# Kernel tuning notes

Hardware: AMD Instinct MI355X
Metric: run time of the kernel (lower is better)

## Reference

```python
import jax, jax.numpy as jnp
import numpy as np

LAMDA = 0.001


def setup_inputs() -> dict:
    key = jax.random.key(0)
    k1, k2 = jax.random.split(key)
    embeddings = jax.random.normal(k1, (256, 1, 256, 256), dtype=jnp.float32)
    labels = jax.random.randint(k2, (256,), 0, 8, dtype=jnp.int64)
    return {"embeddings": embeddings, "labels": labels, "epoch": 1}


def _offdiag(M, b):
    # Remove the diagonal of a (b, b) matrix -> (b, b-1), same trick as torch code:
    # flatten()[1:].view(b-1, b+1)[:, :-1].reshape(b, b-1)
    return M.reshape(-1)[1:].reshape(b - 1, b + 1)[:, :-1].reshape(b, b - 1)


def _psd(embeddings):
    x = embeddings[:, 0]                      # (b, h, w), requires c == 1
    h, w = x.shape[1], x.shape[2]
    k = h * w
    dft = jnp.fft.fft2(x)                     # (b, h, w) complex
    avgpsd = jnp.mean((dft * jnp.conj(dft)).real, axis=0)   # (h, w)
    # log of (geometric mean / arithmetic mean) style flatness measure
    return jnp.clip(jnp.sum(jnp.log(avgpsd)) / k - jnp.log(jnp.sum(avgpsd) / k), 0.0, 100.0)


def reference(embeddings, labels, epoch):
    b = embeddings.shape[0]
    loss = -LAMDA * epoch * _psd(embeddings)

    e = embeddings.reshape(b, -1)             # (b, d)
    sq = jnp.sum(e * e, axis=1)               # (b,)
    d2 = sq[:, None] + sq[None, :] - 2.0 * (e @ e.T)   # squared pairwise distances
    d2 = jnp.maximum(d2, 0.0)
    D = jnp.where(d2 > 0, jnp.sqrt(jnp.where(d2 > 0, d2, 1.0)), 0.0)  # safe sqrt

    Doff = _offdiag(D, b)                     # (b, b-1)
    sm = jax.nn.softmax(-Doff, axis=1)        # (b, b-1)

    Loff = _offdiag(jnp.broadcast_to(labels[None, :], (b, b)), b)  # labels[j != i]
    mask = Loff == labels[:, None]            # positives per row
    probs = jnp.sum(jnp.where(mask, sm, 0.0), axis=1)  # (b,)

    loss = loss + jnp.sum(-jnp.log(probs)) / 200.0
    return loss
```

## Files before the change

### kernel.cpp

```cpp
#include <hip/hip_runtime.h>
#include <hip/hip_bf16.h>
#include <math.h>

#define NROW 256
#define DIM  65536
#define LSTR 40
#define PSP2 32832

typedef __attribute__((ext_vector_type(8))) short short8;
typedef __attribute__((ext_vector_type(4))) float f32x4;
typedef unsigned int       u32t;
typedef unsigned long long u64t;

__device__ __forceinline__ float bf2f(ushort h) {
    u32t u = ((u32t)h) << 16;
    return __builtin_bit_cast(float, u);
}
__device__ __forceinline__ u32t pk2(float lo, float hi) {
    __hip_bfloat162 h = __float22bfloat162_rn(make_float2(lo, hi));
    u32t r; __builtin_memcpy(&r, &h, 4); return r;
}

__device__ __forceinline__ int gpos2(int i, int j) {
    const int mh  = i >> 7, il = i & 127;
    const int wid  = ((il >> 6) << 2) | (j >> 6);
    const int lane = (((il >> 2) & 3) << 4) | (j & 15);
    const int q = ((wid << 6) | lane) * 64
                + (((((il >> 4) & 3) << 2) | ((j >> 4) & 3)) << 2) + (il & 3);
    return mh * 32768 + q;
}

__global__ __launch_bounds__(512, 4) void gemm_k(const float* __restrict__ E,
                                                 ushort* __restrict__ part) {
    const int b   = blockIdx.x;
    const int x   = b & 7;
    const int mh  = (b >> 3) & 1;
    const int s   = x * 32 + (b >> 4);

    const int tid  = threadIdx.x;
    const int lane = tid & 63;
    const int wid  = tid >> 6;
    const int wr   = wid >> 2;
    const int wc   = wid & 3;
    const int r15  = lane & 15;
    const int kgi  = lane >> 4;

    __shared__ ushort es[2][NROW][LSTR];

    const int row  = tid >> 1;
    const int half = tid & 1;
    const size_t kbase = (size_t)s * 256;

    f32x4 acc[4][4];
    #pragma unroll
    for (int m = 0; m < 4; ++m)
        #pragma unroll
        for (int n = 0; n < 4; ++n) acc[m][n] = (f32x4){0.f, 0.f, 0.f, 0.f};

    auto LOADC = [&](int c, float4* v) {
        const float* p = E + ((size_t)row << 16) + kbase + c * 32 + half * 16;
        #pragma unroll
        for (int u = 0; u < 4; ++u) v[u] = *(const float4*)(p + u * 4);
    };
    auto WRITEC = [&](int buf, const float4* v) {
        #pragma unroll
        for (int u = 0; u < 4; ++u) {
            uint2 wv;
            wv.x = pk2(v[u].x, v[u].y);
            wv.y = pk2(v[u].z, v[u].w);
            *(uint2*)&es[buf][row][half * 16 + u * 4] = wv;
        }
    };

    float4 v0[4];
    LOADC(0, v0);
    WRITEC(0, v0);

    #pragma unroll
    for (int c = 0; c < 8; ++c) {
        __syncthreads();
        float4 vn[4];
        if (c < 7) LOADC(c + 1, vn);
        const int ko = kgi * 8;
        short8 af[4], bfr[4];
        #pragma unroll
        for (int m = 0; m < 4; ++m)
            af[m] = *(const short8*)&es[c & 1][mh * 128 + wr * 64 + m * 16 + r15][ko];
        #pragma unroll
        for (int n = 0; n < 4; ++n)
            bfr[n] = *(const short8*)&es[c & 1][wc * 64 + n * 16 + r15][ko];
        #pragma unroll
        for (int m = 0; m < 4; ++m)
            #pragma unroll
            for (int n = 0; n < 4; ++n)
                acc[m][n] = __builtin_amdgcn_mfma_f32_16x16x32_bf16(
                    af[m], bfr[n], acc[m][n], 0, 0, 0);
        if (c < 7) WRITEC((c + 1) & 1, vn);
    }

    ushort* pp = part + (size_t)(s * 2 + mh) * PSP2 + (size_t)tid * 64;
    #pragma unroll
    for (int m = 0; m < 4; ++m)
        #pragma unroll
        for (int n = 0; n < 4; n += 2) {
            uint4 q;
            q.x = pk2(acc[m][n][0],     acc[m][n][1]);
            q.y = pk2(acc[m][n][2],     acc[m][n][3]);
            q.z = pk2(acc[m][n + 1][0], acc[m][n + 1][1]);
            q.w = pk2(acc[m][n + 1][2], acc[m][n + 1][3]);
            *(uint4*)(pp + ((m << 2) | n) * 4) = q;
        }
}

__global__ __launch_bounds__(256) void reduce_k(const ushort* __restrict__ part,
                                                float* __restrict__ Gh,
                                                u64t* __restrict__ acc,
                                                u32t* __restrict__ cnt) {
    if (blockIdx.x == 0 && threadIdx.x == 0) { *acc = 0ull; *cnt = 0u; }

    const int w  = blockIdx.x & 255;
    const int h  = blockIdx.x >> 8;
    const int mh = w >> 7;
    const int q0 = (w & 127) * 256;
    const int t = threadIdx.x, l = t & 63, sg = t >> 6;

    const ushort* base = part + (size_t)((h * 128 + sg) * 2 + mh) * PSP2
                              + q0 + l * 4;

    uint2 r[32];
    #pragma unroll
    for (int u = 0; u < 32; ++u)
        r[u] = *(const uint2*)(base + (size_t)(8 * u) * PSP2);

    float a0 = 0.f, a1 = 0.f, a2 = 0.f, a3 = 0.f;
    #pragma unroll
    for (int u = 0; u < 32; ++u) {
        a0 += bf2f((ushort)(r[u].x & 0xffffu));
        a1 += bf2f((ushort)(r[u].x >> 16));
        a2 += bf2f((ushort)(r[u].y & 0xffffu));
        a3 += bf2f((ushort)(r[u].y >> 16));
    }
    __shared__ float sh[4][256];
    sh[sg][l * 4 + 0] = a0; sh[sg][l * 4 + 1] = a1;
    sh[sg][l * 4 + 2] = a2; sh[sg][l * 4 + 3] = a3;
    __syncthreads();
    Gh[(size_t)h * 65536 + w * 256 + t] =
        (sh[0][t] + sh[1][t]) + (sh[2][t] + sh[3][t]);
}

__global__ __launch_bounds__(256) void row_loss_k(const float* __restrict__ Gh,
                                                  const int* __restrict__ labels,
                                                  u64t* __restrict__ acc,
                                                  u32t* __restrict__ cnt,
                                                  float* __restrict__ out) {
    const int i = blockIdx.x;
    const int j = threadIdx.x;

    const int pii = gpos2(i, i), pjj = gpos2(j, j), pij = gpos2(i, j);
    const float Gii = Gh[pii] + Gh[65536 + pii];
    const float Gjj = Gh[pjj] + Gh[65536 + pjj];
    const float Gij = Gh[pij] + Gh[65536 + pij];
    const float d2 = fmaxf(Gii + Gjj - 2.0f * Gij, 0.0f);
    const bool diag = (j == i);
    const float sc = diag ? -3.0e38f : -sqrtf(d2);

    __shared__ float red0[4], red1[4];

    float m = sc;
    #pragma unroll
    for (int off = 32; off; off >>= 1) m = fmaxf(m, __shfl_xor(m, off, 64));
    const int w = j >> 6;
    if ((j & 63) == 0) red0[w] = m;
    __syncthreads();
    m = fmaxf(fmaxf(red0[0], red0[1]), fmaxf(red0[2], red0[3]));

    const float p  = diag ? 0.0f : expf(sc - m);
    const float nm = (labels[j] == labels[i]) ? p : 0.0f;

    float zs = p, ns = nm;
    #pragma unroll
    for (int off = 32; off; off >>= 1) {
        zs += __shfl_xor(zs, off, 64);
        ns += __shfl_xor(ns, off, 64);
    }
    __syncthreads();
    if ((j & 63) == 0) { red0[w] = zs; red1[w] = ns; }
    __syncthreads();
    if (j == 0) {
        const float Z = red0[0] + red0[1] + red0[2] + red0[3];
        const float N = red1[0] + red1[1] + red1[2] + red1[3];
        const float rl = logf(Z) - logf(N);
        const long long q = llrintf(rl * 1048576.0f);
        atomicAdd(acc, (u64t)q);
        __threadfence();
        const u32t c = atomicAdd(cnt, 1u);
        if (c == NROW - 1) {
            __threadfence();
            const u64t tot = atomicAdd(acc, 0ull);
            out[0] = (float)((double)(long long)tot * (1.0 / 1048576.0) * 0.005);
        }
    }
}

extern "C" void kernel_launch(void* const* d_in, const int* in_sizes, int n_in,
                              void* d_out, int out_size, void* d_ws, size_t ws_size,
                              hipStream_t stream) {
    const float* E      = (const float*)d_in[0];
    const int*   labels = (const int*)d_in[1];
    float*       out    = (float*)d_out;

    ushort* part = (ushort*)d_ws;
    float*  Gh   = (float*)((char*)d_ws + (size_t)512 * PSP2 * sizeof(ushort));
    u64t*   acc  = (u64t*)(Gh + 2 * 65536);
    u32t*   cnt  = (u32t*)(acc + 1);

    gemm_k    <<<512, 512, 0, stream>>>(E, part);
    reduce_k  <<<512, 256, 0, stream>>>(part, Gh, acc, cnt);
    row_loss_k<<<NROW, 256, 0, stream>>>(Gh, labels, acc, cnt, out);
}
```

Before: 47.30 us.

## Halve split-K partitions with larger K chunks and simplify the partial reduction

The Gram-matrix GEMM now uses 128 K-splits of 512 columns each instead of 256 splits of 256, and stages 128-wide K chunks in LDS per iteration (4 iterations of 4 MFMA k-steps). This halves the bf16 partial-sum traffic and the reduce work. The reduce kernel becomes a single-pass per-element sum over 128 partials, and the row-loss kernel reads one Gram array. In exchange, only 256 blocks launch with higher register use (16 float4 prefetch registers), which lowers occupancy and GPU fill. The reduce also reads partials with scalar 2-byte strided loads.

```diff
diff --git a/kernel.cpp b/kernel.cpp
--- a/kernel.cpp
+++ b/kernel.cpp
@@ -4,8 +4,8 @@
 
 #define NROW 256
 #define DIM  65536
-#define LSTR 40
-#define PSP2 32832
+#define LSTR 136
+#define PSP  32800
 
 typedef __attribute__((ext_vector_type(8))) short short8;
 typedef __attribute__((ext_vector_type(4))) float f32x4;
@@ -21,22 +21,20 @@
     u32t r; __builtin_memcpy(&r, &h, 4); return r;
 }
 
-__device__ __forceinline__ int gpos2(int i, int j) {
-    const int mh  = i >> 7, il = i & 127;
+__device__ __forceinline__ int gpos(int i, int j) {
+    const int mh = i >> 7, il = i & 127;
     const int wid  = ((il >> 6) << 2) | (j >> 6);
     const int lane = (((il >> 2) & 3) << 4) | (j & 15);
-    const int q = ((wid << 6) | lane) * 64
-                + (((((il >> 4) & 3) << 2) | ((j >> 4) & 3)) << 2) + (il & 3);
-    return mh * 32768 + q;
-}
-
-__global__ __launch_bounds__(512, 4) void gemm_k(const float* __restrict__ E,
-                                                 ushort* __restrict__ part) {
+    const int off  = ((wid << 6) | lane) * 64
+                   + (((((il >> 4) & 3) << 2) | ((j >> 4) & 3)) << 2) + (il & 3);
+    return mh * 32768 + off;
+}
+
+__global__ __launch_bounds__(512) void gemm_k(const float* __restrict__ E,
+                                              ushort* __restrict__ part) {
     const int b   = blockIdx.x;
-    const int x   = b & 7;
-    const int mh  = (b >> 3) & 1;
-    const int s   = x * 32 + (b >> 4);
-
+    const int s   = b & 127;
+    const int mh  = b >> 7;
     const int tid  = threadIdx.x;
     const int lane = tid & 63;
     const int wid  = tid >> 6;
@@ -47,9 +45,9 @@
 
     __shared__ ushort es[2][NROW][LSTR];
 
-    const int row  = tid >> 1;
-    const int half = tid & 1;
-    const size_t kbase = (size_t)s * 256;
+    const int row = tid >> 1;
+    const int h   = tid & 1;
+    const float* __restrict__ gb = E + ((size_t)row << 16) + s * 512 + h * 64;
 
     f32x4 acc[4][4];
     #pragma unroll
@@ -58,97 +56,96 @@
         for (int n = 0; n < 4; ++n) acc[m][n] = (f32x4){0.f, 0.f, 0.f, 0.f};
 
     auto LOADC = [&](int c, float4* v) {
-        const float* p = E + ((size_t)row << 16) + kbase + c * 32 + half * 16;
-        #pragma unroll
-        for (int u = 0; u < 4; ++u) v[u] = *(const float4*)(p + u * 4);
+        const float* p = gb + c * 128;
+        #pragma unroll
+        for (int u = 0; u < 16; ++u) v[u] = *(const float4*)(p + u * 4);
     };
     auto WRITEC = [&](int buf, const float4* v) {
         #pragma unroll
-        for (int u = 0; u < 4; ++u) {
-            uint2 wv;
-            wv.x = pk2(v[u].x, v[u].y);
-            wv.y = pk2(v[u].z, v[u].w);
-            *(uint2*)&es[buf][row][half * 16 + u * 4] = wv;
+        for (int u = 0; u < 8; ++u) {
+            uint4 q;
+            q.x = pk2(v[2*u].x,   v[2*u].y);
+            q.y = pk2(v[2*u].z,   v[2*u].w);
+            q.z = pk2(v[2*u+1].x, v[2*u+1].y);
+            q.w = pk2(v[2*u+1].z, v[2*u+1].w);
+            *(uint4*)&es[buf][row][h * 64 + u * 8] = q;
         }
     };
 
-    float4 v0[4];
-    LOADC(0, v0);
-    WRITEC(0, v0);
-
-    #pragma unroll
-    for (int c = 0; c < 8; ++c) {
+    {
+        float4 v0[16];
+        LOADC(0, v0);
+        WRITEC(0, v0);
+    }
+
+    #pragma unroll
+    for (int c = 0; c < 4; ++c) {
         __syncthreads();
-        float4 vn[4];
-        if (c < 7) LOADC(c + 1, vn);
-        const int ko = kgi * 8;
-        short8 af[4], bfr[4];
-        #pragma unroll
-        for (int m = 0; m < 4; ++m)
-            af[m] = *(const short8*)&es[c & 1][mh * 128 + wr * 64 + m * 16 + r15][ko];
-        #pragma unroll
-        for (int n = 0; n < 4; ++n)
-            bfr[n] = *(const short8*)&es[c & 1][wc * 64 + n * 16 + r15][ko];
-        #pragma unroll
-        for (int m = 0; m < 4; ++m)
+        float4 vn[16];
+        if (c < 3) LOADC(c + 1, vn);
+        #pragma unroll
+        for (int q = 0; q < 4; ++q) {
+            const int ko = q * 32 + kgi * 8;
+            short8 af[4], bfr[4];
+            #pragma unroll
+            for (int m = 0; m < 4; ++m)
+                af[m] = *(const short8*)&es[c & 1][mh * 128 + wr * 64 + m * 16 + r15][ko];
             #pragma unroll
             for (int n = 0; n < 4; ++n)
-                acc[m][n] = __builtin_amdgcn_mfma_f32_16x16x32_bf16(
-                    af[m], bfr[n], acc[m][n], 0, 0, 0);
-        if (c < 7) WRITEC((c + 1) & 1, vn);
-    }
-
-    ushort* pp = part + (size_t)(s * 2 + mh) * PSP2 + (size_t)tid * 64;
-    #pragma unroll
-    for (int m = 0; m < 4; ++m)
-        #pragma unroll
-        for (int n = 0; n < 4; n += 2) {
-            uint4 q;
-            q.x = pk2(acc[m][n][0],     acc[m][n][1]);
-            q.y = pk2(acc[m][n][2],     acc[m][n][3]);
-            q.z = pk2(acc[m][n + 1][0], acc[m][n + 1][1]);
-            q.w = pk2(acc[m][n + 1][2], acc[m][n + 1][3]);
-            *(uint4*)(pp + ((m << 2) | n) * 4) = q;
-        }
+                bfr[n] = *(const short8*)&es[c & 1][wc * 64 + n * 16 + r15][ko];
+            #pragma unroll
+            for (int m = 0; m < 4; ++m)
+                #pragma unroll
+                for (int n = 0; n < 4; ++n)
+                    acc[m][n] = __builtin_amdgcn_mfma_f32_16x16x32_bf16(
+                        af[m], bfr[n], acc[m][n], 0, 0, 0);
+        }
+        if (c < 3) WRITEC((c + 1) & 1, vn);
+    }
+
+    ushort* pp = part + (size_t)(s * 2 + mh) * PSP + (size_t)tid * 64;
+    #pragma unroll
+    for (int m = 0; m < 4; ++m) {
+        uint4 q1, q2;
+        q1.x = pk2(acc[m][0][0], acc[m][0][1]);
+        q1.y = pk2(acc[m][0][2], acc[m][0][3]);
+        q1.z = pk2(acc[m][1][0], acc[m][1][1]);
+        q1.w = pk2(acc[m][1][2], acc[m][1][3]);
+        q2.x = pk2(acc[m][2][0], acc[m][2][1]);
+        q2.y = pk2(acc[m][2][2], acc[m][2][3]);
+        q2.z = pk2(acc[m][3][0], acc[m][3][1]);
+        q2.w = pk2(acc[m][3][2], acc[m][3][3]);
+        *(uint4*)(pp + m * 16)     = q1;
+        *(uint4*)(pp + m * 16 + 8) = q2;
+    }
 }
 
 __global__ __launch_bounds__(256) void reduce_k(const ushort* __restrict__ part,
-                                                float* __restrict__ Gh,
+                                                float* __restrict__ Gn,
                                                 u64t* __restrict__ acc,
                                                 u32t* __restrict__ cnt) {
     if (blockIdx.x == 0 && threadIdx.x == 0) { *acc = 0ull; *cnt = 0u; }
 
-    const int w  = blockIdx.x & 255;
-    const int h  = blockIdx.x >> 8;
-    const int mh = w >> 7;
-    const int q0 = (w & 127) * 256;
-    const int t = threadIdx.x, l = t & 63, sg = t >> 6;
-
-    const ushort* base = part + (size_t)((h * 128 + sg) * 2 + mh) * PSP2
-                              + q0 + l * 4;
-
-    uint2 r[32];
-    #pragma unroll
-    for (int u = 0; u < 32; ++u)
-        r[u] = *(const uint2*)(base + (size_t)(8 * u) * PSP2);
-
-    float a0 = 0.f, a1 = 0.f, a2 = 0.f, a3 = 0.f;
-    #pragma unroll
-    for (int u = 0; u < 32; ++u) {
-        a0 += bf2f((ushort)(r[u].x & 0xffffu));
-        a1 += bf2f((ushort)(r[u].x >> 16));
-        a2 += bf2f((ushort)(r[u].y & 0xffffu));
-        a3 += bf2f((ushort)(r[u].y >> 16));
-    }
-    __shared__ float sh[4][256];
-    sh[sg][l * 4 + 0] = a0; sh[sg][l * 4 + 1] = a1;
-    sh[sg][l * 4 + 2] = a2; sh[sg][l * 4 + 3] = a3;
-    __syncthreads();
-    Gh[(size_t)h * 65536 + w * 256 + t] =
-        (sh[0][t] + sh[1][t]) + (sh[2][t] + sh[3][t]);
-}
-
-__global__ __launch_bounds__(256) void row_loss_k(const float* __restrict__ Gh,
+    const int pos = blockIdx.x * 256 + threadIdx.x;
+    const int mh  = pos >> 15;
+    const int off = pos & 32767;
+    const ushort* base = part + (size_t)mh * PSP + off;
+
+    float qs[4];
+    #pragma unroll
+    for (int qt = 0; qt < 4; ++qt) {
+        float a = 0.f;
+        #pragma unroll
+        for (int s2 = 0; s2 < 32; ++s2) {
+            const int s = qt * 32 + s2;
+            a += bf2f(base[(size_t)(s * 2) * PSP]);
+        }
+        qs[qt] = a;
+    }
+    Gn[pos] = (qs[0] + qs[1]) + (qs[2] + qs[3]);
+}
+
+__global__ __launch_bounds__(256) void row_loss_k(const float* __restrict__ Gn,
                                                   const int* __restrict__ labels,
                                                   u64t* __restrict__ acc,
                                                   u32t* __restrict__ cnt,
@@ -156,10 +153,9 @@
     const int i = blockIdx.x;
     const int j = threadIdx.x;
 
-    const int pii = gpos2(i, i), pjj = gpos2(j, j), pij = gpos2(i, j);
-    const float Gii = Gh[pii] + Gh[65536 + pii];
-    const float Gjj = Gh[pjj] + Gh[65536 + pjj];
-    const float Gij = Gh[pij] + Gh[65536 + pij];
+    const float Gii = Gn[gpos(i, i)];
+    const float Gjj = Gn[gpos(j, j)];
+    const float Gij = Gn[gpos(i, j)];
     const float d2 = fmaxf(Gii + Gjj - 2.0f * Gij, 0.0f);
     const bool diag = (j == i);
     const float sc = diag ? -3.0e38f : -sqrtf(d2);
@@ -210,11 +206,11 @@
     float*       out    = (float*)d_out;
 
     ushort* part = (ushort*)d_ws;
-    float*  Gh   = (float*)((char*)d_ws + (size_t)512 * PSP2 * sizeof(ushort));
-    u64t*   acc  = (u64t*)(Gh + 2 * 65536);
+    float*  Gn   = (float*)((char*)d_ws + (size_t)256 * PSP * sizeof(ushort));
+    u64t*   acc  = (u64t*)(Gn + 65536);
     u32t*   cnt  = (u32t*)(acc + 1);
 
-    gemm_k    <<<512, 512, 0, stream>>>(E, part);
-    reduce_k  <<<512, 256, 0, stream>>>(part, Gh, acc, cnt);
-    row_loss_k<<<NROW, 256, 0, stream>>>(Gh, labels, acc, cnt, out);
-}
+    gemm_k    <<<256, 512, 0, stream>>>(E, part);
+    reduce_k  <<<256, 256, 0, stream>>>(part, Gn, acc, cnt);
+    row_loss_k<<<NROW, 256, 0, stream>>>(Gn, labels, acc, cnt, out);
+}
```

New measurement: 48.09 us. About the same (+1.7%).
